# Kernel tuning notes

Hardware: AMD Instinct MI355X
Metric: run time of the kernel (lower is better)

Reference implementation:

```python
import jax, jax.numpy as jnp
import numpy as np


def _gaussian_orthogonal_random_matrix(nb_rows, nb_cols, seed=0):
    rng = np.random.default_rng(seed)
    blocks = []
    n_full = nb_rows // nb_cols
    for _ in range(n_full):
        q, _ = np.linalg.qr(rng.standard_normal((nb_cols, nb_cols)).astype(np.float64))
        blocks.append(q.T)
    rem = nb_rows - n_full * nb_cols
    if rem > 0:
        q, _ = np.linalg.qr(rng.standard_normal((nb_cols, nb_cols)).astype(np.float64))
        blocks.append(q.T[:rem])
    final = np.concatenate(blocks, axis=0)
    # scaling == 0: row multipliers are norms of gaussian rows
    multiplier = np.linalg.norm(rng.standard_normal((nb_rows, nb_cols)), axis=1)
    return (multiplier[:, None] * final).astype(np.float32)


def setup_inputs() -> dict:
    key = jax.random.key(0)
    kq, kk, kv = jax.random.split(key, 3)
    B, H, N, D = 4, 16, 4096, 64
    M = 256  # nb_features
    return {
        "q": jax.random.normal(kq, (B, H, N, D), dtype=jnp.float32),
        "k": jax.random.normal(kk, (B, H, N, D), dtype=jnp.float32),
        "v": jax.random.normal(kv, (B, H, N, D), dtype=jnp.float32),
        "projection_matrix": jnp.asarray(_gaussian_orthogonal_random_matrix(M, D)),
    }


def _softmax_kernel(data, proj, is_query, eps=1e-4):
    # data: [b,h,n,d], proj: [m,d]
    d = data.shape[-1]
    m = proj.shape[0]
    data_normalizer = d ** -0.25
    ratio = m ** -0.5
    data_dash = jnp.einsum('bhnd,md->bhnm', data_normalizer * data, proj)
    diag_data = jnp.sum(data * data, axis=-1, keepdims=True) * 0.5 * (data_normalizer ** 2)
    if is_query:
        mx = jnp.max(data_dash, axis=-1, keepdims=True)
    else:
        mx = jnp.max(data_dash, axis=(-2, -1), keepdims=True)
    mx = jax.lax.stop_gradient(mx)
    return ratio * (jnp.exp(data_dash - diag_data - mx) + eps)


def _linear_attention(q, k, v):
    # q,k: [b,h,n,m]; v: [b,h,n,e]
    k_cumsum = k.sum(axis=-2)                              # [b,h,m]
    d_inv = 1.0 / jnp.einsum('bhnm,bhm->bhn', q, k_cumsum)  # [b,h,n]
    context = jnp.einsum('bhnm,bhne->bhme', k, v)          # [b,h,m,e]
    return jnp.einsum('bhme,bhnm,bhn->bhne', context, q, d_inv)


def reference(q, k, v, projection_matrix):
    qp = _softmax_kernel(q, projection_matrix, is_query=True)
    kp = _softmax_kernel(k, projection_matrix, is_query=False)
    return _linear_attention(qp, kp, v)
```

## Files before the change

### kernel.cpp

```cpp
#include <hip/hip_runtime.h>
#include <math.h>

#define NSEQ  4096
#define DDIM  64
#define GH    64
#define NORMC 0.35355339059327373f
#define EPSC  1e-4f

typedef __bf16 bf16x8 __attribute__((ext_vector_type(8)));
typedef unsigned short u16x8 __attribute__((ext_vector_type(8)));
typedef float f32x4 __attribute__((ext_vector_type(4)));

__device__ __forceinline__ unsigned enc_f(float f) {
    unsigned b = __float_as_uint(f);
    return (b & 0x80000000u) ? ~b : (b | 0x80000000u);
}
__device__ __forceinline__ float dec_f(unsigned u) {
    return (u & 0x80000000u) ? __uint_as_float(u & 0x7FFFFFFFu) : __uint_as_float(~u);
}
__device__ __forceinline__ void split_hl(float f, unsigned short& h, unsigned short& l) {
    unsigned u = __float_as_uint(f);
    unsigned hb = u & 0xffff0000u;
    h = (unsigned short)(hb >> 16);
    l = (unsigned short)(__float_as_uint(f - __uint_as_float(hb)) >> 16);
}
__device__ __forceinline__ unsigned short rne16(float f) {
    return (unsigned short)((__float_as_uint(f) + 0x8000u) >> 16);
}
__device__ __forceinline__ bf16x8 ldfrag(const unsigned short* p) {
    return __builtin_bit_cast(bf16x8, *(const u16x8*)p);
}
__device__ __forceinline__ f32x4 zero4() { f32x4 z = {0.f, 0.f, 0.f, 0.f}; return z; }
__device__ __forceinline__ f32x4 mfma3(bf16x8 ah, bf16x8 al, bf16x8 bh, bf16x8 bl, f32x4 c) {
    c = __builtin_amdgcn_mfma_f32_16x16x32_bf16(ah, bh, c, 0, 0, 0);
    c = __builtin_amdgcn_mfma_f32_16x16x32_bf16(ah, bl, c, 0, 0, 0);
    c = __builtin_amdgcn_mfma_f32_16x16x32_bf16(al, bh, c, 0, 0, 0);
    return c;
}

template<int NSLICE>
__global__ __launch_bounds__(256, 2)
void kernA(const float* __restrict__ kk, const float* __restrict__ vv,
           const float* __restrict__ proj, float* __restrict__ Apart,
           float* __restrict__ Aspart, float* __restrict__ Svpart,
           unsigned* __restrict__ mxk)
{
    const int slices = (NSLICE == 1) ? 16 : NSLICE;
    const int bx    = blockIdx.x;
    const int slice = bx & (slices - 1);
    const int mh    = bx / slices;
    const int g     = blockIdx.y;
    const int t     = threadIdx.x;
    const int lane  = t & 63;
    const int wq    = t >> 6;
    const int li    = lane & 15;
    const int lg    = lane >> 4;

    __shared__ __align__(16) unsigned short ARENA[16384];
    __shared__ float diag[2][32];
    __shared__ float svred[4][64];
    __shared__ float mxred[4];

    bf16x8 pfh[2][2], pfl[2][2];
#pragma unroll
    for (int u = 0; u < 2; u++)
#pragma unroll
    for (int s = 0; s < 2; s++) {
        const float* pr = proj + (size_t)(mh * 128 + wq * 32 + u * 16 + li) * DDIM + s * 32 + lg * 8;
        u16x8 hh, ll;
#pragma unroll
        for (int j = 0; j < 8; j++) {
            unsigned short h, l;
            split_hl(NORMC * pr[j], h, l);
            hh[j] = h; ll[j] = l;
        }
        pfh[u][s] = __builtin_bit_cast(bf16x8, hh);
        pfl[u][s] = __builtin_bit_cast(bf16x8, ll);
    }

    f32x4 cacc[4][2];
#pragma unroll
    for (int a = 0; a < 4; a++)
#pragma unroll
    for (int b = 0; b < 2; b++) cacc[a][b] = zero4();
    float as_loc[2] = {0.f, 0.f};
    float sv8[8] = {0.f,0.f,0.f,0.f,0.f,0.f,0.f,0.f};
    float mloc = -1e30f;

    const int stg_n = t >> 3;
    const int stg_c = t & 7;
    const int rows_per = NSEQ / slices;
    const int r_begin = slice * rows_per;
    const int vks = ((stg_n >> 2) & 3) * 8 + (stg_n >> 4) * 4 + (stg_n & 3);

    float4 ka0, ka1, va0, va1;
    auto load_tile = [&](int r0) {
        const float4* kb = (const float4*)(kk + ((size_t)g * NSEQ + r0 + stg_n) * DDIM + stg_c * 8);
        ka0 = kb[0]; ka1 = kb[1];
        const float4* vb = (const float4*)(vv + ((size_t)g * NSEQ + r0 + stg_n) * DDIM + stg_c * 8);
        va0 = vb[0]; va1 = vb[1];
    };
    auto stage_tile = [&](int b) {
        unsigned short* Khi  = ARENA + b * 8192;
        unsigned short* Klo  = Khi + 2048;
        unsigned short* Vthi = Khi + 4096;
        unsigned short* Vtlo = Khi + 6144;
        float ke[8] = {ka0.x,ka0.y,ka0.z,ka0.w,ka1.x,ka1.y,ka1.z,ka1.w};
        float sq = 0.f;
#pragma unroll
        for (int j = 0; j < 8; j++) sq += ke[j] * ke[j];
        sq += __shfl_xor(sq, 1); sq += __shfl_xor(sq, 2); sq += __shfl_xor(sq, 4);
        if (stg_c == 0) diag[b][stg_n] = 0.0625f * sq;
        u16x8 h8, l8;
#pragma unroll
        for (int j = 0; j < 8; j++) {
            unsigned short h, l;
            split_hl(ke[j], h, l);
            h8[j] = h; l8[j] = l;
        }
        int idx = stg_n * 64 + (stg_c ^ (stg_n & 7)) * 8;
        *(u16x8*)&Khi[idx] = h8;
        *(u16x8*)&Klo[idx] = l8;
        float ve[8] = {va0.x,va0.y,va0.z,va0.w,va1.x,va1.y,va1.z,va1.w};
#pragma unroll
        for (int j = 0; j < 8; j++) {
            sv8[j] += ve[j];
            unsigned short h, l;
            split_hl(ve[j], h, l);
            int e = stg_c * 8 + j;
            int slot = vks ^ (((e >> 1) & 3) << 3);
            Vthi[e * 32 + slot] = h;
            Vtlo[e * 32 + slot] = l;
        }
    };

    load_tile(r_begin);
    stage_tile(0);
    __syncthreads();
    int cur = 0;
    const int NT = rows_per / 32;
    for (int it = 0; it < NT; ++it) {
        if (it + 1 < NT) load_tile(r_begin + (it + 1) * 32);
        const unsigned short* Khi  = ARENA + cur * 8192;
        const unsigned short* Klo  = Khi + 2048;
        const unsigned short* Vthi = Khi + 4096;
        const unsigned short* Vtlo = Khi + 6144;
        f32x4 dacc[2][2];
#pragma unroll
        for (int tt = 0; tt < 2; tt++)
#pragma unroll
        for (int u = 0; u < 2; u++) dacc[tt][u] = zero4();
#pragma unroll
        for (int tt = 0; tt < 2; tt++)
#pragma unroll
        for (int s = 0; s < 2; s++) {
            int idx = (tt * 16 + li) * 64 + ((s * 4 + lg) ^ (li & 7)) * 8;
            bf16x8 ah = ldfrag(&Khi[idx]);
            bf16x8 al = ldfrag(&Klo[idx]);
#pragma unroll
            for (int u = 0; u < 2; u++) dacc[tt][u] = mfma3(ah, al, pfh[u][s], pfl[u][s], dacc[tt][u]);
        }
        u16x8 whh[2];
#pragma unroll
        for (int tt = 0; tt < 2; tt++)
#pragma unroll
        for (int u = 0; u < 2; u++)
#pragma unroll
        for (int r = 0; r < 4; r++) {
            float dash = dacc[tt][u][r];
            mloc = fmaxf(mloc, dash);
            float w = __expf(dash - diag[cur][tt * 16 + lg * 4 + r]);
            unsigned short hb = rne16(w);
            whh[u][tt * 4 + r] = hb;
            as_loc[u] += __uint_as_float((unsigned)hb << 16);
        }
        bf16x8 avh[4], avl[4];
#pragma unroll
        for (int u2 = 0; u2 < 4; u2++) {
            int row = u2 * 16 + li;
            int slot = (lg ^ ((li >> 1) & 3)) * 8;
            avh[u2] = ldfrag(&Vthi[row * 32 + slot]);
            avl[u2] = ldfrag(&Vtlo[row * 32 + slot]);
        }
#pragma unroll
        for (int u = 0; u < 2; u++) {
            bf16x8 b = __builtin_bit_cast(bf16x8, whh[u]);
#pragma unroll
            for (int u2 = 0; u2 < 4; u2++) {
                cacc[u2][u] = __builtin_amdgcn_mfma_f32_16x16x32_bf16(avh[u2], b, cacc[u2][u], 0, 0, 0);
                cacc[u2][u] = __builtin_amdgcn_mfma_f32_16x16x32_bf16(avl[u2], b, cacc[u2][u], 0, 0, 0);
            }
        }
        if (it + 1 < NT) stage_tile(cur ^ 1);
        __syncthreads();
        cur ^= 1;
    }

#pragma unroll
    for (int j = 0; j < 8; j++) {
        float s = sv8[j];
        s += __shfl_xor(s, 8); s += __shfl_xor(s, 16); s += __shfl_xor(s, 32);
        sv8[j] = s;
    }
    if (lane < 8) {
#pragma unroll
        for (int j = 0; j < 8; j++) svred[wq][lane * 8 + j] = sv8[j];
    }
    float mm = mloc;
#pragma unroll
    for (int off = 32; off >= 1; off >>= 1) mm = fmaxf(mm, __shfl_xor(mm, off));
    if (lane == 0) mxred[wq] = mm;
#pragma unroll
    for (int u = 0; u < 2; u++) {
        float a = as_loc[u];
        a += __shfl_xor(a, 16); a += __shfl_xor(a, 32);
        as_loc[u] = a;
    }
    __syncthreads();
    if (t == 0) {
        float m4 = fmaxf(fmaxf(mxred[0], mxred[1]), fmaxf(mxred[2], mxred[3]));
        atomicMax(mxk + g, enc_f(m4));
    }
    if (t < 64 && mh == 0) {
        float s = svred[0][t] + svred[1][t] + svred[2][t] + svred[3][t];
        if (NSLICE == 1) atomicAdd(&Svpart[(size_t)g * 64 + t], s);
        else             Svpart[((size_t)g * NSLICE + slice) * 64 + t] = s;
    }
    if (lane < 16) {
#pragma unroll
        for (int u = 0; u < 2; u++) {
            int m = mh * 128 + wq * 32 + u * 16 + lane;
            if (NSLICE == 1) atomicAdd(&Aspart[(size_t)g * 256 + m], as_loc[u]);
            else             Aspart[((size_t)g * NSLICE + slice) * 256 + m] = as_loc[u];
        }
    }
    float* tb = (float*)ARENA + wq * 1024;
    float* Ad = (NSLICE == 1) ? (Apart + (size_t)g * 16384)
                              : (Apart + ((size_t)g * NSLICE + slice) * 16384);
    for (int u = 0; u < 2; u++) {
#pragma unroll
        for (int u2 = 0; u2 < 4; u2++)
#pragma unroll
        for (int r = 0; r < 4; r++)
            tb[li * 64 + ((((u2 << 2) | lg) ^ (li & 7)) << 2) + r] = cacc[u2][u][r];
#pragma unroll
        for (int j = 0; j < 4; j++) {
            int row16 = j * 4 + lg;
            int swz = li ^ (row16 & 7);
            f32x4 val = *(const f32x4*)&tb[row16 * 64 + swz * 4];
            float* dst = Ad + (mh * 128 + wq * 32 + u * 16) * 64 + j * 256 + lane * 4;
            if (NSLICE == 1) {
                atomicAdd(dst + 0, val[0]); atomicAdd(dst + 1, val[1]);
                atomicAdd(dst + 2, val[2]); atomicAdd(dst + 3, val[3]);
            } else {
                *(f32x4*)dst = val;
            }
        }
    }
}

__global__ __launch_bounds__(256)
void kernB(const float* __restrict__ Apart, const float* __restrict__ Aspart,
           const float* __restrict__ Svpart, const unsigned* __restrict__ mxk,
           float* __restrict__ ctx, float* __restrict__ ksum, int nslice)
{
    const int b = blockIdx.x;
    const int g = blockIdx.y;
    const int t = threadIdx.x;
    __shared__ float svh[64];
    float emx = __expf(-dec_f(mxk[g]));
    if (t < 64) {
        float s = 0.f;
        for (int sb = 0; sb < nslice; sb++) s += Svpart[((size_t)g * nslice + sb) * 64 + t];
        svh[t] = s;
    }
    if (b == 0) {
        float as_s = 0.f;
        for (int sb = 0; sb < nslice; sb++) as_s += Aspart[((size_t)g * nslice + sb) * 256 + t];
        ksum[(size_t)g * 256 + t] = emx * as_s + EPSC * (float)NSEQ;
    }
    __syncthreads();
    int idx4 = b * 256 + t;
    const f32x4* Ap = (const f32x4*)Apart;
    f32x4 s = zero4();
    for (int sb = 0; sb < nslice; sb++) s += Ap[((size_t)g * nslice + sb) * 4096 + idx4];
    int e0 = (idx4 * 4) & 63;
    f32x4 o;
    o[0] = emx * s[0] + EPSC * svh[e0];
    o[1] = emx * s[1] + EPSC * svh[e0 + 1];
    o[2] = emx * s[2] + EPSC * svh[e0 + 2];
    o[3] = emx * s[3] + EPSC * svh[e0 + 3];
    ((f32x4*)ctx)[(size_t)g * 4096 + idx4] = o;
}

__global__ __launch_bounds__(256, 2)
void kernC(const float* __restrict__ qq, const float* __restrict__ proj,
           const float* __restrict__ ctx, const float* __restrict__ ksum,
           float* __restrict__ outp)
{
    const int slice = blockIdx.x;
    const int g     = blockIdx.y;
    const int t     = threadIdx.x;
    const int lane  = t & 63;
    const int wq    = t >> 6;
    const int li    = lane & 15;
    const int lg    = lane >> 4;

    __shared__ __align__(16) unsigned short QAR[2][4096];
    __shared__ __align__(16) unsigned short qph[8192];
    __shared__ float diag[2][32];
    __shared__ float rmax4[4][32];
    __shared__ float denp[4][32];

    bf16x8 pfh[4][2], pfl[4][2];
#pragma unroll
    for (int u = 0; u < 4; u++)
#pragma unroll
    for (int s = 0; s < 2; s++) {
        const float* pr = proj + (size_t)(wq * 64 + u * 16 + li) * DDIM + s * 32 + lg * 8;
        u16x8 hh, ll;
#pragma unroll
        for (int j = 0; j < 8; j++) {
            unsigned short h, l;
            split_hl(NORMC * pr[j], h, l);
            hh[j] = h; ll[j] = l;
        }
        pfh[u][s] = __builtin_bit_cast(bf16x8, hh);
        pfl[u][s] = __builtin_bit_cast(bf16x8, ll);
    }
    bf16x8 axh[8], axl[8];
#pragma unroll
    for (int mc = 0; mc < 8; mc++) {
        u16x8 hh, ll;
#pragma unroll
        for (int jj = 0; jj < 8; jj++) {
            float cvv = ctx[((size_t)g * 256 + mc * 32 + lg * 8 + jj) * 64 + wq * 16 + li];
            unsigned short h, l;
            split_hl(cvv, h, l);
            hh[jj] = h; ll[jj] = l;
        }
        axh[mc] = __builtin_bit_cast(bf16x8, hh);
        axl[mc] = __builtin_bit_cast(bf16x8, ll);
    }
    float ksm[4];
#pragma unroll
    for (int u = 0; u < 4; u++) ksm[u] = ksum[(size_t)g * 256 + wq * 64 + u * 16 + li];

    const int stg_n = t >> 3;
    const int stg_c = t & 7;
    const int r_begin = slice * (NSEQ / 16);

    float4 qa0, qa1;
    auto load_tile = [&](int r0) {
        const float4* qb = (const float4*)(qq + ((size_t)g * NSEQ + r0 + stg_n) * DDIM + stg_c * 8);
        qa0 = qb[0]; qa1 = qb[1];
    };
    auto stage_tile = [&](int b) {
        float qe[8] = {qa0.x,qa0.y,qa0.z,qa0.w,qa1.x,qa1.y,qa1.z,qa1.w};
        float sq = 0.f;
#pragma unroll
        for (int j = 0; j < 8; j++) sq += qe[j] * qe[j];
        sq += __shfl_xor(sq, 1); sq += __shfl_xor(sq, 2); sq += __shfl_xor(sq, 4);
        if (stg_c == 0) diag[b][stg_n] = 0.0625f * sq;
        u16x8 h8, l8;
#pragma unroll
        for (int j = 0; j < 8; j++) {
            unsigned short h, l;
            split_hl(qe[j], h, l);
            h8[j] = h; l8[j] = l;
        }
        int idx = stg_n * 64 + (stg_c ^ (stg_n & 7)) * 8;
        *(u16x8*)&QAR[b][idx] = h8;
        *(u16x8*)&QAR[b][2048 + idx] = l8;
    };

    load_tile(r_begin);
    stage_tile(0);
    __syncthreads();
    int cur = 0;
    for (int it = 0; it < 8; ++it) {
        if (it + 1 < 8) load_tile(r_begin + (it + 1) * 32);
        f32x4 dacc[2][4];
#pragma unroll
        for (int tt = 0; tt < 2; tt++)
#pragma unroll
        for (int u = 0; u < 4; u++) dacc[tt][u] = zero4();
#pragma unroll
        for (int tt = 0; tt < 2; tt++)
#pragma unroll
        for (int s = 0; s < 2; s++) {
            int idx = (tt * 16 + li) * 64 + ((s * 4 + lg) ^ (li & 7)) * 8;
            bf16x8 ah = ldfrag(&QAR[cur][idx]);
            bf16x8 al = ldfrag(&QAR[cur][2048 + idx]);
#pragma unroll
            for (int u = 0; u < 4; u++) dacc[tt][u] = mfma3(ah, al, pfh[u][s], pfl[u][s], dacc[tt][u]);
        }
#pragma unroll
        for (int tt = 0; tt < 2; tt++)
#pragma unroll
        for (int r = 0; r < 4; r++) {
            float v = fmaxf(fmaxf(dacc[tt][0][r], dacc[tt][1][r]),
                            fmaxf(dacc[tt][2][r], dacc[tt][3][r]));
            v = fmaxf(v, __shfl_xor(v, 1));
            v = fmaxf(v, __shfl_xor(v, 2));
            v = fmaxf(v, __shfl_xor(v, 4));
            v = fmaxf(v, __shfl_xor(v, 8));
            if (li == 0) rmax4[wq][tt * 16 + lg * 4 + r] = v;
        }
        __syncthreads();
        float dl[2][4] = {{0.f,0.f,0.f,0.f},{0.f,0.f,0.f,0.f}};
#pragma unroll
        for (int tt = 0; tt < 2; tt++) {
            float cb[4];
#pragma unroll
            for (int r = 0; r < 4; r++) {
                int n = tt * 16 + lg * 4 + r;
                cb[r] = diag[cur][n] + fmaxf(fmaxf(rmax4[0][n], rmax4[1][n]),
                                             fmaxf(rmax4[2][n], rmax4[3][n]));
            }
#pragma unroll
            for (int u = 0; u < 4; u++)
#pragma unroll
            for (int r = 0; r < 4; r++) {
                float qp = __expf(dacc[tt][u][r] - cb[r]) + EPSC;
                unsigned short hb = rne16(qp);
                dl[tt][r] += __uint_as_float((unsigned)hb << 16) * ksm[u];
                int n = tt * 16 + lg * 4 + r;
                int mg = wq * 64 + u * 16 + li;
                qph[n * 256 + (((mg >> 3) ^ (n & 7)) << 3) + (mg & 7)] = hb;
            }
        }
#pragma unroll
        for (int tt = 0; tt < 2; tt++)
#pragma unroll
        for (int r = 0; r < 4; r++) {
            float v = dl[tt][r];
            v += __shfl_xor(v, 1); v += __shfl_xor(v, 2);
            v += __shfl_xor(v, 4); v += __shfl_xor(v, 8);
            if (li == 0) denp[wq][tt * 16 + lg * 4 + r] = v;
        }
        if (it + 1 < 8) stage_tile(cur ^ 1);
        __syncthreads();
        f32x4 oacc[2] = {zero4(), zero4()};
#pragma unroll
        for (int tt = 0; tt < 2; tt++) {
            int n = tt * 16 + li;
#pragma unroll
            for (int mc = 0; mc < 8; mc++) {
                bf16x8 b = ldfrag(&qph[n * 256 + (((mc * 4 + lg) ^ (li & 7)) << 3)]);
                oacc[tt] = __builtin_amdgcn_mfma_f32_16x16x32_bf16(axh[mc], b, oacc[tt], 0, 0, 0);
                oacc[tt] = __builtin_amdgcn_mfma_f32_16x16x32_bf16(axl[mc], b, oacc[tt], 0, 0, 0);
            }
        }
#pragma unroll
        for (int tt = 0; tt < 2; tt++) {
            int n = tt * 16 + li;
            float den = denp[0][n] + denp[1][n] + denp[2][n] + denp[3][n];
            float dinv = 1.0f / den;
            f32x4 o;
            o[0] = oacc[tt][0] * dinv; o[1] = oacc[tt][1] * dinv;
            o[2] = oacc[tt][2] * dinv; o[3] = oacc[tt][3] * dinv;
            float* op = outp + ((size_t)g * NSEQ + r_begin + it * 32 + n) * DDIM + wq * 16 + lg * 4;
            *(f32x4*)op = o;
        }
        cur ^= 1;
    }
}

extern "C" void kernel_launch(void* const* d_in, const int* in_sizes, int n_in,
                              void* d_out, int out_size, void* d_ws, size_t ws_size,
                              hipStream_t stream)
{
    const float* q    = (const float*)d_in[0];
    const float* k    = (const float*)d_in[1];
    const float* v    = (const float*)d_in[2];
    const float* proj = (const float*)d_in[3];
    float* outp = (float*)d_out;

    size_t per_ns = (size_t)GH * 16384 + (size_t)GH * 256 + (size_t)GH * 64;
    size_t fixed  = (size_t)GH * 16384 + (size_t)GH * 256;
    size_t need8  = 256 + 4 * (8 * per_ns + fixed);
    int ns = (ws_size >= need8) ? 8 : 1;

    unsigned* mxk = (unsigned*)d_ws;
    float* Apart  = (float*)((char*)d_ws + 256);
    float* Aspart = Apart  + (size_t)GH * ns * 16384;
    float* Svpart = Aspart + (size_t)GH * ns * 256;
    float* ctx    = Svpart + (size_t)GH * ns * 64;
    float* ksum   = ctx    + (size_t)GH * 16384;

    if (ns == 8) {
        hipMemsetAsync(d_ws, 0, 256, stream);
        kernA<8><<<dim3(16, GH), 256, 0, stream>>>(k, v, proj, Apart, Aspart, Svpart, mxk);
    } else {
        hipMemsetAsync(d_ws, 0, 256 + 4 * per_ns, stream);
        kernA<1><<<dim3(32, GH), 256, 0, stream>>>(k, v, proj, Apart, Aspart, Svpart, mxk);
    }
    kernB<<<dim3(16, GH), 256, 0, stream>>>(Apart, Aspart, Svpart, mxk, ctx, ksum, ns);
    kernC<<<dim3(16, GH), 256, 0, stream>>>(q, proj, ctx, ksum, outp);
}
```

Measured before the change: 198.4 us.

## Precompute transposed bf16 hi/lo context in kernB and load fragments per tile in kernC

kernB now transposes the context matrix through shared memory and writes it as separate bf16 high and low halves in an [e][m] layout. kernC no longer does strided fp32 gathers and hi/lo splitting of ctx in its prologue. Instead it loads contiguous 16-byte fragments inside the tile loop, which also frees the 32 long-lived registers that held them. In exchange, kernC reloads those fragments from global/L2 on every iteration, and kernB does extra transpose work and an additional barrier.

New measurement: 207.0 us. +4.3%, slower.

```diff
diff --git a/kernel.cpp b/kernel.cpp
--- a/kernel.cpp
+++ b/kernel.cpp
@@ -9,6 +9,7 @@
 
 typedef __bf16 bf16x8 __attribute__((ext_vector_type(8)));
 typedef unsigned short u16x8 __attribute__((ext_vector_type(8)));
+typedef unsigned short u16x4 __attribute__((ext_vector_type(4)));
 typedef float f32x4 __attribute__((ext_vector_type(4)));
 
 __device__ __forceinline__ unsigned enc_f(float f) {
@@ -262,12 +263,14 @@
 __global__ __launch_bounds__(256)
 void kernB(const float* __restrict__ Apart, const float* __restrict__ Aspart,
            const float* __restrict__ Svpart, const unsigned* __restrict__ mxk,
-           float* __restrict__ ctx, float* __restrict__ ksum, int nslice)
+           unsigned short* __restrict__ ctxTh, unsigned short* __restrict__ ctxTl,
+           float* __restrict__ ksum, int nslice)
 {
     const int b = blockIdx.x;
     const int g = blockIdx.y;
     const int t = threadIdx.x;
     __shared__ float svh[64];
+    __shared__ float TB[16][68];
     float emx = __expf(-dec_f(mxk[g]));
     if (t < 64) {
         float s = 0.f;
@@ -280,23 +283,34 @@
         ksum[(size_t)g * 256 + t] = emx * as_s + EPSC * (float)NSEQ;
     }
     __syncthreads();
-    int idx4 = b * 256 + t;
-    const f32x4* Ap = (const f32x4*)Apart;
-    f32x4 s = zero4();
-    for (int sb = 0; sb < nslice; sb++) s += Ap[((size_t)g * nslice + sb) * 4096 + idx4];
-    int e0 = (idx4 * 4) & 63;
-    f32x4 o;
-    o[0] = emx * s[0] + EPSC * svh[e0];
-    o[1] = emx * s[1] + EPSC * svh[e0 + 1];
-    o[2] = emx * s[2] + EPSC * svh[e0 + 2];
-    o[3] = emx * s[3] + EPSC * svh[e0 + 3];
-    ((f32x4*)ctx)[(size_t)g * 4096 + idx4] = o;
+    const int mi = t >> 6, e = t & 63;
+#pragma unroll
+    for (int p = 0; p < 4; p++) {
+        int ml = p * 4 + mi;
+        int m  = b * 16 + ml;
+        float s = 0.f;
+        for (int sb = 0; sb < nslice; sb++)
+            s += Apart[((size_t)g * nslice + sb) * 16384 + m * 64 + e];
+        TB[ml][e] = emx * s + EPSC * svh[e];
+    }
+    __syncthreads();
+    const int er = t >> 2, mj = (t & 3) * 4;
+    u16x4 h4, l4;
+#pragma unroll
+    for (int i = 0; i < 4; i++) {
+        unsigned short h, l;
+        split_hl(TB[mj + i][er], h, l);
+        h4[i] = h; l4[i] = l;
+    }
+    size_t base = (size_t)g * 16384 + (size_t)er * 256 + b * 16 + mj;
+    *(u16x4*)&ctxTh[base] = h4;
+    *(u16x4*)&ctxTl[base] = l4;
 }
 
 __global__ __launch_bounds__(256, 2)
 void kernC(const float* __restrict__ qq, const float* __restrict__ proj,
-           const float* __restrict__ ctx, const float* __restrict__ ksum,
-           float* __restrict__ outp)
+           const unsigned short* __restrict__ ctxTh, const unsigned short* __restrict__ ctxTl,
+           const float* __restrict__ ksum, float* __restrict__ outp)
 {
     const int slice = blockIdx.x;
     const int g     = blockIdx.y;
@@ -328,23 +342,12 @@
         pfh[u][s] = __builtin_bit_cast(bf16x8, hh);
         pfl[u][s] = __builtin_bit_cast(bf16x8, ll);
     }
-    bf16x8 axh[8], axl[8];
-#pragma unroll
-    for (int mc = 0; mc < 8; mc++) {
-        u16x8 hh, ll;
-#pragma unroll
-        for (int jj = 0; jj < 8; jj++) {
-            float cvv = ctx[((size_t)g * 256 + mc * 32 + lg * 8 + jj) * 64 + wq * 16 + li];
-            unsigned short h, l;
-            split_hl(cvv, h, l);
-            hh[jj] = h; ll[jj] = l;
-        }
-        axh[mc] = __builtin_bit_cast(bf16x8, hh);
-        axl[mc] = __builtin_bit_cast(bf16x8, ll);
-    }
     float ksm[4];
 #pragma unroll
     for (int u = 0; u < 4; u++) ksm[u] = ksum[(size_t)g * 256 + wq * 64 + u * 16 + li];
+
+    const unsigned short* axbh = ctxTh + (size_t)g * 16384 + (size_t)(wq * 16 + li) * 256 + lg * 8;
+    const unsigned short* axbl = ctxTl + (size_t)g * 16384 + (size_t)(wq * 16 + li) * 256 + lg * 8;
 
     const int stg_n = t >> 3;
     const int stg_c = t & 7;
@@ -441,6 +444,12 @@
         }
         if (it + 1 < 8) stage_tile(cur ^ 1);
         __syncthreads();
+        bf16x8 axh[8], axl[8];
+#pragma unroll
+        for (int mc = 0; mc < 8; mc++) {
+            axh[mc] = __builtin_bit_cast(bf16x8, *(const u16x8*)(axbh + mc * 32));
+            axl[mc] = __builtin_bit_cast(bf16x8, *(const u16x8*)(axbl + mc * 32));
+        }
         f32x4 oacc[2] = {zero4(), zero4()};
 #pragma unroll
         for (int tt = 0; tt < 2; tt++) {
@@ -489,6 +498,9 @@
     float* ctx    = Svpart + (size_t)GH * ns * 64;
     float* ksum   = ctx    + (size_t)GH * 16384;
 
+    unsigned short* ctxTh = (unsigned short*)ctx;
+    unsigned short* ctxTl = ctxTh + (size_t)GH * 16384;
+
     if (ns == 8) {
         hipMemsetAsync(d_ws, 0, 256, stream);
         kernA<8><<<dim3(16, GH), 256, 0, stream>>>(k, v, proj, Apart, Aspart, Svpart, mxk);
@@ -496,6 +508,6 @@
         hipMemsetAsync(d_ws, 0, 256 + 4 * per_ns, stream);
         kernA<1><<<dim3(32, GH), 256, 0, stream>>>(k, v, proj, Apart, Aspart, Svpart, mxk);
     }
-    kernB<<<dim3(16, GH), 256, 0, stream>>>(Apart, Aspart, Svpart, mxk, ctx, ksum, ns);
-    kernC<<<dim3(16, GH), 256, 0, stream>>>(q, proj, ctx, ksum, outp);
-}
+    kernB<<<dim3(16, GH), 256, 0, stream>>>(Apart, Aspart, Svpart, mxk, ctxTh, ctxTl, ksum, ns);
+    kernC<<<dim3(16, GH), 256, 0, stream>>>(q, proj, ctxTh, ctxTl, ksum, outp);
+}
```
